# Performance work log

Hardware: AMD Instinct MI355X
Metric: run time of the kernel (lower is better)

Reference implementation:

```python
import jax, jax.numpy as jnp
import numpy as np

D_K = 128
SCALER = np.sqrt(D_K).astype(np.float32)

def setup_inputs() -> dict:
    key = jax.random.key(0)
    kq, kk, kv = jax.random.split(key, 3)
    B, L, D = 16, 2048, D_K
    q = jax.random.normal(kq, (B, L, D), dtype=jnp.float32)
    k = jax.random.normal(kk, (B, L, D), dtype=jnp.float32)
    v = jax.random.normal(kv, (B, L, D), dtype=jnp.float32)
    return {"q": q, "k": k, "v": v}

def reference(q, k, v):
    # score[b, i, j] = q[b, i, :] . k[b, j, :] / sqrt(d_k)
    score = jnp.einsum('bid,bjd->bij', q, k) / SCALER
    attn = jax.nn.softmax(score, axis=-1)
    # output[b, i, :] = sum_j attn[b, i, j] * v[b, j, :]
    return jnp.einsum('bij,bjd->bid', attn, v)
```

## Files before the change

kernel.cpp:

```cpp
#include <hip/hip_runtime.h>
#include <stdint.h>


typedef short bf16x8 __attribute__((ext_vector_type(8)));
typedef float f32x4 __attribute__((ext_vector_type(4)));
typedef unsigned int u32;
typedef unsigned short u16;

#define L_SEQ  2048
#define D_HEAD 128
#define NIT    16
#define TSZ    8388608u
#define PART_SZ (512u * 32768u)
#define LSUM_OFF (2u * TSZ + PART_SZ)
#define WS_NEED (LSUM_OFF + 512u * 128u * 4u)

__device__ __forceinline__ unsigned pk2(float lo, float hi) {
    union { float f; unsigned u; } a, b;
    a.f = lo; b.f = hi;
    return __builtin_amdgcn_perm(b.u + 0x8000u, a.u + 0x8000u, 0x07060302u);
}
__device__ __forceinline__ float ex2(float x) { return __builtin_amdgcn_exp2f(x); }
__device__ __forceinline__ float bflo(unsigned w) {
    union { unsigned u; float f; } v; v.u = w << 16; return v.f;
}
__device__ __forceinline__ float bfhi(unsigned w) {
    union { unsigned u; float f; } v; v.u = w & 0xffff0000u; return v.f;
}
__device__ __forceinline__ void gl_lds16(const u16* g, u16* l) {
    __builtin_amdgcn_global_load_lds(
        (const __attribute__((address_space(1))) u32*)g,
        (__attribute__((address_space(3))) u32*)l, 16, 0, 0);
}

__global__ __launch_bounds__(256, 4)
void prepass(const float* __restrict__ K, const float* __restrict__ V,
             u16* __restrict__ kb, u16* __restrict__ vt) {
    const int id = blockIdx.x, t = threadIdx.x;
    if (id < 512) {
        const float* src = K + (size_t)id * 64 * 128;
        u16*        dst = kb + (size_t)id * 64 * 128;
        const int r = t >> 2;
        #pragma unroll
        for (int i = 0; i < 4; ++i) {
            int gp = (t & 3) * 4 + i;
            int gs = gp ^ (r & 7);
            const float* s = src + r * 128 + gs * 8;
            float4 x0 = *(const float4*)s, x1 = *(const float4*)(s + 4);
            uint4 w;
            w.x = pk2(x0.x, x0.y); w.y = pk2(x0.z, x0.w);
            w.z = pk2(x1.x, x1.y); w.w = pk2(x1.z, x1.w);
            *(uint4*)(dst + r * 128 + gp * 8) = w;
        }
    } else {
        __shared__ float vl[64 * 132];
        const int bid = id - 512;
        const float* src = V + (size_t)bid * 64 * 128;
        {
            int r = t >> 2, c0 = (t & 3) * 32;
            #pragma unroll
            for (int j = 0; j < 8; ++j)
                *(float4*)(&vl[r * 132 + c0 + j * 4]) =
                    *(const float4*)(src + r * 128 + c0 + j * 4);
        }
        __syncthreads();
        u16* dst = vt + (size_t)bid * 8192;
        const int d = t >> 1;
        #pragma unroll
        for (int i = 0; i < 4; ++i) {
            int gp = (t & 1) * 4 + i;
            int kvb = (gp ^ (d & 7)) * 8;
            float p[8];
            #pragma unroll
            for (int j = 0; j < 8; ++j) p[j] = vl[(kvb + j) * 132 + d];
            uint4 w;
            w.x = pk2(p[0], p[1]); w.y = pk2(p[2], p[3]);
            w.z = pk2(p[4], p[5]); w.w = pk2(p[6], p[7]);
            *(uint4*)(dst + d * 64 + gp * 8) = w;
        }
    }
}

__global__ __launch_bounds__(256, 2)
void attn_split(const float* __restrict__ Qg, const u16* __restrict__ kb,
                const u16* __restrict__ vt, u16* __restrict__ part,
                float* __restrict__ lsum) {
    __shared__ __align__(16) char smem[51200];
    const int tid = threadIdx.x;
    const int wv = tid >> 6, lane = tid & 63;
    const int c = lane & 15, qd = lane >> 4, cx = c & 7;
    const int bid = blockIdx.x;
    const int p = bid >> 1, kvh = bid & 1;
    const int b = p & 15, qblk = p >> 4;

    const float* Qp = Qg + (size_t)b * L_SEQ * D_HEAD;
    const u16*   Kp = kb + (size_t)b * L_SEQ * D_HEAD + (size_t)kvh * 1024 * 128;
    const u16*   Vp = vt + (size_t)b * 32 * 8192 + (size_t)kvh * 16 * 8192;
    u16* Kl = (u16*)smem;
    u16* Vl = (u16*)(smem + 16384);
    u16* Pl = (u16*)(smem + 32768) + wv * 2304;

    const int so = wv * 2048 + lane * 8;

    #pragma unroll
    for (int i = 0; i < 4; ++i) {
        gl_lds16(Kp + so + i * 512, Kl + so + i * 512);
        gl_lds16(Vp + so + i * 512, Vl + so + i * 512);
    }

    const float QS = 1.4426950408889634f / 11.313708498984761f;
    bf16x8 qf[2][4];
    #pragma unroll
    for (int s = 0; s < 2; ++s) {
        const float* qrow = Qp + (size_t)(qblk * 128 + wv * 32 + s * 16 + c) * 128 + qd * 8;
        #pragma unroll
        for (int kt = 0; kt < 4; ++kt) {
            float4 x0 = *(const float4*)(qrow + kt * 32);
            float4 x1 = *(const float4*)(qrow + kt * 32 + 4);
            union { unsigned u[4]; bf16x8 v; } tt;
            tt.u[0] = pk2(x0.x * QS, x0.y * QS);
            tt.u[1] = pk2(x0.z * QS, x0.w * QS);
            tt.u[2] = pk2(x1.x * QS, x1.y * QS);
            tt.u[3] = pk2(x1.z * QS, x1.w * QS);
            qf[s][kt] = tt.v;
        }
    }

    f32x4 acc[2][8];
    #pragma unroll
    for (int s = 0; s < 2; ++s)
        #pragma unroll
        for (int dt = 0; dt < 8; ++dt) acc[s][dt] = (f32x4){0.f, 0.f, 0.f, 0.f};
    float lrun[2] = {0.f, 0.f};

    __syncthreads();

    for (int it = 0; it < NIT; ++it) {
        f32x4 st[4][2];
        #pragma unroll
        for (int v = 0; v < 4; ++v) {
            st[v][0] = (f32x4){0.f, 0.f, 0.f, 0.f};
            st[v][1] = (f32x4){0.f, 0.f, 0.f, 0.f};
        }
        #pragma unroll
        for (int kt = 0; kt < 4; ++kt) {
            const int g = ((kt * 4 + qd) ^ cx) * 8;
            #pragma unroll
            for (int v = 0; v < 4; ++v) {
                bf16x8 a = *(const bf16x8*)(Kl + (v * 16 + c) * 128 + g);
                st[v][0] = __builtin_amdgcn_mfma_f32_16x16x32_bf16(a, qf[0][kt], st[v][0], 0, 0, 0);
                st[v][1] = __builtin_amdgcn_mfma_f32_16x16x32_bf16(a, qf[1][kt], st[v][1], 0, 0, 0);
            }
        }
        __syncthreads();

        if (it + 1 < NIT) {
            const u16* kg = Kp + (size_t)(it + 1) * 8192 + so;
            #pragma unroll
            for (int i = 0; i < 4; ++i) gl_lds16(kg + i * 512, Kl + so + i * 512);
        }

        #pragma unroll
        for (int s = 0; s < 2; ++s) {
            float lsm = 0.f;
            #pragma unroll
            for (int v = 0; v < 4; ++v) {
                float p0 = ex2(st[v][s].x), p1 = ex2(st[v][s].y);
                float p2 = ex2(st[v][s].z), p3 = ex2(st[v][s].w);
                lsm += (p0 + p1) + (p2 + p3);
                uint2 w; w.x = pk2(p0, p1); w.y = pk2(p2, p3);
                *(uint2*)(Pl + (s * 16 + c) * 72 + v * 16 + qd * 4) = w;
            }
            lrun[s] += lsm;
        }
        bf16x8 pf[2][2];
        #pragma unroll
        for (int h = 0; h < 2; ++h)
            #pragma unroll
            for (int s = 0; s < 2; ++s)
                pf[h][s] = *(const bf16x8*)(Pl + (s * 16 + c) * 72 + h * 32 + qd * 8);

        #pragma unroll
        for (int dt = 0; dt < 8; ++dt) {
            #pragma unroll
            for (int h = 0; h < 2; ++h) {
                bf16x8 a = *(const bf16x8*)(Vl + (dt * 16 + c) * 64 + ((h * 4 + qd) ^ cx) * 8);
                acc[0][dt] = __builtin_amdgcn_mfma_f32_16x16x32_bf16(a, pf[h][0], acc[0][dt], 0, 0, 0);
                acc[1][dt] = __builtin_amdgcn_mfma_f32_16x16x32_bf16(a, pf[h][1], acc[1][dt], 0, 0, 0);
            }
        }
        __syncthreads();

        if (it + 1 < NIT) {
            const u16* vg = Vp + (size_t)(it + 1) * 8192 + so;
            #pragma unroll
            for (int i = 0; i < 4; ++i) gl_lds16(vg + i * 512, Vl + so + i * 512);
        }
    }

    float ls[2];
    #pragma unroll
    for (int s = 0; s < 2; ++s) {
        float l = lrun[s];
        l += __shfl_xor(l, 16);
        l += __shfl_xor(l, 32);
        ls[s] = l;
    }
    u16* pb = part + (size_t)bid * 16384;
    #pragma unroll
    for (int s = 0; s < 2; ++s)
        #pragma unroll
        for (int dt = 0; dt < 8; ++dt) {
            f32x4 o = acc[s][dt];
            uint2 w; w.x = pk2(o.x, o.y); w.y = pk2(o.z, o.w);
            *(uint2*)(pb + ((((wv * 2 + s) * 8 + dt) * 64 + lane) << 2)) = w;
        }
    if (qd == 0) {
        lsum[p * 256 + kvh * 128 + wv * 32 + c]      = ls[0];
        lsum[p * 256 + kvh * 128 + wv * 32 + 16 + c] = ls[1];
    }
}

__global__ __launch_bounds__(256, 2)
void combine(const u16* __restrict__ part, const float* __restrict__ lsum,
             float* __restrict__ Og) {
    __shared__ float inv[128];
    __shared__ __align__(16) float Ol[64 * 132];
    const int t = threadIdx.x, p = blockIdx.x;
    const int b = p & 15, qblk = p >> 4;
    if (t < 128) {
        float la = lsum[p * 256 + t], lb = lsum[p * 256 + 128 + t];
        inv[t] = 1.0f / (la + lb);
    }
    const uint2* A = (const uint2*)(part + (size_t)(2 * p) * 16384);
    const uint2* B = (const uint2*)(part + (size_t)(2 * p + 1) * 16384);
    __syncthreads();
    #pragma unroll
    for (int h = 0; h < 2; ++h) {
        #pragma unroll
        for (int i = 0; i < 8; ++i) {
            int slot = i * 256 + t;
            int lc = slot >> 6, lane = slot & 63;
            int gc = h * 32 + lc;
            int s = (lc >> 3) & 1, dt = lc & 7;
            int qd = lane >> 4, c = lane & 15;
            int row = (lc >> 4) * 32 + s * 16 + c;
            int d0 = dt * 16 + qd * 4;
            uint2 wa = A[(size_t)gc * 64 + lane];
            uint2 wb = B[(size_t)gc * 64 + lane];
            float iv = inv[h * 64 + row];
            float4 o;
            o.x = (bflo(wa.x) + bflo(wb.x)) * iv;
            o.y = (bfhi(wa.x) + bfhi(wb.x)) * iv;
            o.z = (bflo(wa.y) + bflo(wb.y)) * iv;
            o.w = (bfhi(wa.y) + bfhi(wb.y)) * iv;
            *(float4*)(&Ol[row * 132 + d0]) = o;
        }
        __syncthreads();
        #pragma unroll
        for (int i = 0; i < 8; ++i) {
            int slot = i * 256 + t;
            int row = slot >> 5, c4 = slot & 31;
            float4 val = *(const float4*)(&Ol[row * 132 + c4 * 4]);
            size_t q = (size_t)b * L_SEQ + qblk * 128 + h * 64 + row;
            *(float4*)(Og + q * D_HEAD + c4 * 4) = val;
        }
        __syncthreads();
    }
}

#define FKST 136
#define FVST 72
#define FPST 72
#define FOST 132
#define FV_OFF  17408
#define FP_OFF  (17408 + 18432)
#define FSMEM   (FP_OFF + 4 * 32 * FPST * 2)

union F4fb { float4 v; float f[4]; };

__global__ __launch_bounds__(256, 1)
void attn_fwd_fb(const float* __restrict__ Qg, const float* __restrict__ Kg,
                 const float* __restrict__ Vg, float* __restrict__ Og) {
    __shared__ __align__(16) char smem[FSMEM];
    unsigned short* Kl = (unsigned short*)(smem);
    unsigned short* Vl = (unsigned short*)(smem + FV_OFF);
    float*          Ol = (float*)smem;

    const int tid  = threadIdx.x;
    const int wv   = tid >> 6;
    const int lane = tid & 63;
    const int c    = lane & 15;
    const int qd   = lane >> 4;
    unsigned short* Pl = (unsigned short*)(smem + FP_OFF) + wv * (32 * FPST);

    const int b  = blockIdx.x & 15;
    const int qb = blockIdx.x >> 4;

    const float* Qb = Qg + (size_t)b * L_SEQ * D_HEAD;
    const float* Kb = Kg + (size_t)b * L_SEQ * D_HEAD;
    const float* Vb = Vg + (size_t)b * L_SEQ * D_HEAD;

    const int krow = tid >> 2, kch = tid & 3;
    const int vcc  = tid & 31, vgk = tid >> 5;

    const float QS = 1.4426950408889634f / 11.313708498984761f;
    bf16x8 qf[2][4];
    #pragma unroll
    for (int s = 0; s < 2; ++s) {
        const float* qrow = Qb + (size_t)(qb * 128 + wv * 32 + s * 16 + c) * D_HEAD + qd * 8;
        #pragma unroll
        for (int kt = 0; kt < 4; ++kt) {
            float4 x0 = *(const float4*)(qrow + kt * 32);
            float4 x1 = *(const float4*)(qrow + kt * 32 + 4);
            union { unsigned u[4]; bf16x8 v; } t;
            t.u[0] = pk2(x0.x * QS, x0.y * QS);
            t.u[1] = pk2(x0.z * QS, x0.w * QS);
            t.u[2] = pk2(x1.x * QS, x1.y * QS);
            t.u[3] = pk2(x1.z * QS, x1.w * QS);
            qf[s][kt] = t.v;
        }
    }

    F4fb kreg[8], vreg[8];
    {
        const float* kp = Kb + (size_t)krow * D_HEAD + kch * 32;
        #pragma unroll
        for (int r = 0; r < 8; ++r) kreg[r].v = *(const float4*)(kp + r * 4);
        const float* vp = Vb + (size_t)(vgk * 8) * D_HEAD + vcc * 4;
        #pragma unroll
        for (int r = 0; r < 8; ++r) vreg[r].v = *(const float4*)(vp + (size_t)r * D_HEAD);
    }

    f32x4 acc[2][8];
    #pragma unroll
    for (int s = 0; s < 2; ++s)
        #pragma unroll
        for (int dt = 0; dt < 8; ++dt) acc[s][dt] = (f32x4){0.f, 0.f, 0.f, 0.f};
    float lrun[2] = {0.f, 0.f};

    for (int it = 0; it < 32; ++it) {
        #pragma unroll
        for (int i = 0; i < 4; ++i) {
            uint4 w;
            w.x = pk2(kreg[2*i].f[0],   kreg[2*i].f[1]);
            w.y = pk2(kreg[2*i].f[2],   kreg[2*i].f[3]);
            w.z = pk2(kreg[2*i+1].f[0], kreg[2*i+1].f[1]);
            w.w = pk2(kreg[2*i+1].f[2], kreg[2*i+1].f[3]);
            *(uint4*)(&Kl[krow * FKST + kch * 32 + i * 8]) = w;
        }
        #pragma unroll
        for (int dd = 0; dd < 4; ++dd) {
            uint4 w;
            w.x = pk2(vreg[0].f[dd], vreg[1].f[dd]);
            w.y = pk2(vreg[2].f[dd], vreg[3].f[dd]);
            w.z = pk2(vreg[4].f[dd], vreg[5].f[dd]);
            w.w = pk2(vreg[6].f[dd], vreg[7].f[dd]);
            *(uint4*)(&Vl[(vcc * 4 + dd) * FVST + vgk * 8]) = w;
        }
        __syncthreads();

        if (it + 1 < 32) {
            const float* kp = Kb + (size_t)((it + 1) * 64 + krow) * D_HEAD + kch * 32;
            #pragma unroll
            for (int r = 0; r < 8; ++r) kreg[r].v = *(const float4*)(kp + r * 4);
            const float* vp = Vb + (size_t)((it + 1) * 64 + vgk * 8) * D_HEAD + vcc * 4;
            #pragma unroll
            for (int r = 0; r < 8; ++r) vreg[r].v = *(const float4*)(vp + (size_t)r * D_HEAD);
        }

        f32x4 st[4][2];
        #pragma unroll
        for (int v = 0; v < 4; ++v) { st[v][0] = (f32x4){0,0,0,0}; st[v][1] = (f32x4){0,0,0,0}; }
        #pragma unroll
        for (int kt = 0; kt < 4; ++kt) {
            #pragma unroll
            for (int v = 0; v < 4; ++v) {
                bf16x8 a = *(const bf16x8*)(&Kl[(v * 16 + c) * FKST + kt * 32 + qd * 8]);
                st[v][0] = __builtin_amdgcn_mfma_f32_16x16x32_bf16(a, qf[0][kt], st[v][0], 0, 0, 0);
                st[v][1] = __builtin_amdgcn_mfma_f32_16x16x32_bf16(a, qf[1][kt], st[v][1], 0, 0, 0);
            }
        }

        #pragma unroll
        for (int s = 0; s < 2; ++s) {
            float lsm = 0.f;
            #pragma unroll
            for (int v = 0; v < 4; ++v) {
                float p0 = ex2(st[v][s].x), p1 = ex2(st[v][s].y);
                float p2 = ex2(st[v][s].z), p3 = ex2(st[v][s].w);
                lsm += (p0 + p1) + (p2 + p3);
                uint2 w; w.x = pk2(p0, p1); w.y = pk2(p2, p3);
                *(uint2*)(&Pl[(s * 16 + c) * FPST + v * 16 + qd * 4]) = w;
            }
            lrun[s] += lsm;
        }
        bf16x8 pf[2][2];
        #pragma unroll
        for (int h = 0; h < 2; ++h)
            #pragma unroll
            for (int s = 0; s < 2; ++s)
                pf[h][s] = *(const bf16x8*)(&Pl[(s * 16 + c) * FPST + h * 32 + qd * 8]);

        #pragma unroll
        for (int dt = 0; dt < 8; ++dt) {
            #pragma unroll
            for (int h = 0; h < 2; ++h) {
                bf16x8 a = *(const bf16x8*)(&Vl[(dt * 16 + c) * FVST + h * 32 + qd * 8]);
                acc[0][dt] = __builtin_amdgcn_mfma_f32_16x16x32_bf16(a, pf[h][0], acc[0][dt], 0, 0, 0);
                acc[1][dt] = __builtin_amdgcn_mfma_f32_16x16x32_bf16(a, pf[h][1], acc[1][dt], 0, 0, 0);
            }
        }
        __syncthreads();
    }

    float inv[2];
    #pragma unroll
    for (int s = 0; s < 2; ++s) {
        float l = lrun[s];
        l += __shfl_xor(l, 16);
        l += __shfl_xor(l, 32);
        inv[s] = 1.0f / l;
    }
    #pragma unroll
    for (int pass = 0; pass < 2; ++pass) {
        if ((wv >> 1) == pass) {
            int rw = (wv & 1) * 32;
            #pragma unroll
            for (int s = 0; s < 2; ++s)
                #pragma unroll
                for (int dt = 0; dt < 8; ++dt) {
                    f32x4 o = acc[s][dt];
                    float4 w = {o.x * inv[s], o.y * inv[s], o.z * inv[s], o.w * inv[s]};
                    *(float4*)(&Ol[(rw + s * 16 + c) * FOST + dt * 16 + qd * 4]) = w;
                }
        }
        __syncthreads();
        #pragma unroll
        for (int i = 0; i < 8; ++i) {
            int idx = i * 256 + tid;
            int row = idx >> 5, c4 = idx & 31;
            float4 val = *(const float4*)(&Ol[row * FOST + c4 * 4]);
            size_t q = (size_t)b * L_SEQ + qb * 128 + pass * 64 + row;
            *(float4*)(Og + q * D_HEAD + c4 * 4) = val;
        }
        __syncthreads();
    }
}

extern "C" void kernel_launch(void* const* d_in, const int* in_sizes, int n_in,
                              void* d_out, int out_size, void* d_ws, size_t ws_size,
                              hipStream_t stream) {
    const float* q = (const float*)d_in[0];
    const float* k = (const float*)d_in[1];
    const float* v = (const float*)d_in[2];
    float* out = (float*)d_out;
    if (ws_size >= (size_t)WS_NEED) {
        u16* kb = (u16*)d_ws;
        u16* vt = (u16*)((char*)d_ws + TSZ);
        u16* part = (u16*)((char*)d_ws + 2 * (size_t)TSZ);
        float* ls = (float*)((char*)d_ws + LSUM_OFF);
        prepass<<<dim3(1024), dim3(256), 0, stream>>>(k, v, kb, vt);
        attn_split<<<dim3(512), dim3(256), 0, stream>>>(q, kb, vt, part, ls);
        combine<<<dim3(256), dim3(256), 0, stream>>>(part, ls, out);
    } else {
        attn_fwd_fb<<<dim3(256), dim3(256), 0, stream>>>(q, k, v, out);
    }
}
```

Before: 142.5 us.

## Use 512-thread attention blocks with 4-way KV split and rewrite V transpose prepass

Adds an attn8 kernel in which each 512-thread block handles 256 query rows against a quarter of the KV sequence, so each K/V tile in LDS is reused by eight waves instead of four. A combine4 kernel merges the four partial outputs. The V transpose in the prepass now packs to bf16 in registers before writing LDS, which halves LDS traffic. The fallback path without a workspace is removed. The risks are heavier partial-result traffic, larger LDS per block and lower occupancy.

```diff
diff --git a/kernel.cpp b/kernel.cpp
--- a/kernel.cpp
+++ b/kernel.cpp
@@ -9,11 +9,13 @@
 
 #define L_SEQ  2048
 #define D_HEAD 128
-#define NIT    16
 #define TSZ    8388608u
-#define PART_SZ (512u * 32768u)
-#define LSUM_OFF (2u * TSZ + PART_SZ)
-#define WS_NEED (LSUM_OFF + 512u * 128u * 4u)
+#define W2_PART (2u * TSZ)
+#define W2_LSUM (W2_PART + 512u * 65536u)
+#define WS_NEED2 (W2_LSUM + 512u * 256u * 4u)
+#define W5_PART (2u * TSZ)
+#define W5_LSUM (W5_PART + 512u * 32768u)
+#define WS_NEED5 (W5_LSUM + 512u * 128u * 4u)
 
 __device__ __forceinline__ unsigned pk2(float lo, float hi) {
     union { float f; unsigned u; } a, b;
@@ -53,31 +55,223 @@
             *(uint4*)(dst + r * 128 + gp * 8) = w;
         }
     } else {
-        __shared__ float vl[64 * 132];
+        __shared__ __align__(16) u16 vl[128 * 72];
         const int bid = id - 512;
         const float* src = V + (size_t)bid * 64 * 128;
-        {
-            int r = t >> 2, c0 = (t & 3) * 32;
-            #pragma unroll
-            for (int j = 0; j < 8; ++j)
-                *(float4*)(&vl[r * 132 + c0 + j * 4]) =
-                    *(const float4*)(src + r * 128 + c0 + j * 4);
+        const int vcc = t & 31, vgk = t >> 5;
+        union { float4 v; float f[4]; } vr[8];
+        const float* vp = src + (size_t)(vgk * 8) * 128 + vcc * 4;
+        #pragma unroll
+        for (int r = 0; r < 8; ++r) vr[r].v = *(const float4*)(vp + (size_t)r * 128);
+        #pragma unroll
+        for (int dd = 0; dd < 4; ++dd) {
+            uint4 w;
+            w.x = pk2(vr[0].f[dd], vr[1].f[dd]);
+            w.y = pk2(vr[2].f[dd], vr[3].f[dd]);
+            w.z = pk2(vr[4].f[dd], vr[5].f[dd]);
+            w.w = pk2(vr[6].f[dd], vr[7].f[dd]);
+            *(uint4*)(&vl[(vcc * 4 + dd) * 72 + vgk * 8]) = w;
         }
         __syncthreads();
         u16* dst = vt + (size_t)bid * 8192;
-        const int d = t >> 1;
         #pragma unroll
         for (int i = 0; i < 4; ++i) {
-            int gp = (t & 1) * 4 + i;
-            int kvb = (gp ^ (d & 7)) * 8;
-            float p[8];
-            #pragma unroll
-            for (int j = 0; j < 8; ++j) p[j] = vl[(kvb + j) * 132 + d];
-            uint4 w;
-            w.x = pk2(p[0], p[1]); w.y = pk2(p[2], p[3]);
-            w.z = pk2(p[4], p[5]); w.w = pk2(p[6], p[7]);
-            *(uint4*)(dst + d * 64 + gp * 8) = w;
-        }
+            int flat = t + 256 * i;
+            int d = flat >> 3, gp = flat & 7;
+            uint4 w = *(const uint4*)(&vl[d * 72 + ((gp ^ (d & 7)) * 8)]);
+            *(uint4*)(dst + (size_t)flat * 8) = w;
+        }
+    }
+}
+
+__global__ __launch_bounds__(512, 4)
+void attn8(const float* __restrict__ Qg, const u16* __restrict__ kb,
+           const u16* __restrict__ vt, u16* __restrict__ part,
+           float* __restrict__ lsum) {
+    __shared__ __align__(16) char smem[69632];
+    const int tid = threadIdx.x;
+    const int wv = tid >> 6, lane = tid & 63;
+    const int c = lane & 15, qd = lane >> 4, cx = c & 7;
+    const int bid = blockIdx.x;
+    const int p = bid >> 2, kvh = bid & 3;
+    const int b = p & 15, qblk = p >> 4;
+
+    const float* Qp = Qg + (size_t)b * L_SEQ * D_HEAD;
+    const u16*   Kp = kb + (size_t)b * L_SEQ * D_HEAD + (size_t)kvh * 512 * 128;
+    const u16*   Vp = vt + (size_t)b * 32 * 8192 + (size_t)kvh * 8 * 8192;
+    u16* Kl = (u16*)smem;
+    u16* Vl = (u16*)(smem + 16384);
+    u16* Pl = (u16*)(smem + 32768) + wv * 2304;
+
+    const int so = tid * 8;
+
+    #pragma unroll
+    for (int i = 0; i < 2; ++i) {
+        gl_lds16(Kp + so + i * 4096, Kl + so + i * 4096);
+        gl_lds16(Vp + so + i * 4096, Vl + so + i * 4096);
+    }
+
+    const float QS = 1.4426950408889634f / 11.313708498984761f;
+    bf16x8 qf[2][4];
+    #pragma unroll
+    for (int s = 0; s < 2; ++s) {
+        const float* qrow = Qp + (size_t)(qblk * 256 + wv * 32 + s * 16 + c) * 128 + qd * 8;
+        #pragma unroll
+        for (int kt = 0; kt < 4; ++kt) {
+            float4 x0 = *(const float4*)(qrow + kt * 32);
+            float4 x1 = *(const float4*)(qrow + kt * 32 + 4);
+            union { unsigned u[4]; bf16x8 v; } tt;
+            tt.u[0] = pk2(x0.x * QS, x0.y * QS);
+            tt.u[1] = pk2(x0.z * QS, x0.w * QS);
+            tt.u[2] = pk2(x1.x * QS, x1.y * QS);
+            tt.u[3] = pk2(x1.z * QS, x1.w * QS);
+            qf[s][kt] = tt.v;
+        }
+    }
+
+    f32x4 acc[2][8];
+    #pragma unroll
+    for (int s = 0; s < 2; ++s)
+        #pragma unroll
+        for (int dt = 0; dt < 8; ++dt) acc[s][dt] = (f32x4){0.f, 0.f, 0.f, 0.f};
+    float lrun[2] = {0.f, 0.f};
+
+    __syncthreads();
+
+    for (int it = 0; it < 8; ++it) {
+        f32x4 st[4][2];
+        #pragma unroll
+        for (int v = 0; v < 4; ++v) {
+            st[v][0] = (f32x4){0.f, 0.f, 0.f, 0.f};
+            st[v][1] = (f32x4){0.f, 0.f, 0.f, 0.f};
+        }
+        #pragma unroll
+        for (int kt = 0; kt < 4; ++kt) {
+            const int g = ((kt * 4 + qd) ^ cx) * 8;
+            #pragma unroll
+            for (int v = 0; v < 4; ++v) {
+                bf16x8 a = *(const bf16x8*)(Kl + (v * 16 + c) * 128 + g);
+                st[v][0] = __builtin_amdgcn_mfma_f32_16x16x32_bf16(a, qf[0][kt], st[v][0], 0, 0, 0);
+                st[v][1] = __builtin_amdgcn_mfma_f32_16x16x32_bf16(a, qf[1][kt], st[v][1], 0, 0, 0);
+            }
+        }
+        __syncthreads();
+
+        if (it + 1 < 8) {
+            const u16* kg = Kp + (size_t)(it + 1) * 8192 + so;
+            #pragma unroll
+            for (int i = 0; i < 2; ++i) gl_lds16(kg + i * 4096, Kl + so + i * 4096);
+        }
+
+        #pragma unroll
+        for (int s = 0; s < 2; ++s) {
+            float lsm = 0.f;
+            #pragma unroll
+            for (int v = 0; v < 4; ++v) {
+                float p0 = ex2(st[v][s].x), p1 = ex2(st[v][s].y);
+                float p2 = ex2(st[v][s].z), p3 = ex2(st[v][s].w);
+                lsm += (p0 + p1) + (p2 + p3);
+                uint2 w; w.x = pk2(p0, p1); w.y = pk2(p2, p3);
+                *(uint2*)(Pl + (s * 16 + c) * 72 + v * 16 + qd * 4) = w;
+            }
+            lrun[s] += lsm;
+        }
+        bf16x8 pf[2][2];
+        #pragma unroll
+        for (int h = 0; h < 2; ++h)
+            #pragma unroll
+            for (int s = 0; s < 2; ++s)
+                pf[h][s] = *(const bf16x8*)(Pl + (s * 16 + c) * 72 + h * 32 + qd * 8);
+
+        #pragma unroll
+        for (int dt = 0; dt < 8; ++dt) {
+            #pragma unroll
+            for (int h = 0; h < 2; ++h) {
+                bf16x8 a = *(const bf16x8*)(Vl + (dt * 16 + c) * 64 + ((h * 4 + qd) ^ cx) * 8);
+                acc[0][dt] = __builtin_amdgcn_mfma_f32_16x16x32_bf16(a, pf[h][0], acc[0][dt], 0, 0, 0);
+                acc[1][dt] = __builtin_amdgcn_mfma_f32_16x16x32_bf16(a, pf[h][1], acc[1][dt], 0, 0, 0);
+            }
+        }
+        __syncthreads();
+
+        if (it + 1 < 8) {
+            const u16* vg = Vp + (size_t)(it + 1) * 8192 + so;
+            #pragma unroll
+            for (int i = 0; i < 2; ++i) gl_lds16(vg + i * 4096, Vl + so + i * 4096);
+        }
+    }
+
+    float ls[2];
+    #pragma unroll
+    for (int s = 0; s < 2; ++s) {
+        float l = lrun[s];
+        l += __shfl_xor(l, 16);
+        l += __shfl_xor(l, 32);
+        ls[s] = l;
+    }
+    u16* pb = part + (size_t)bid * 32768;
+    #pragma unroll
+    for (int s = 0; s < 2; ++s)
+        #pragma unroll
+        for (int dt = 0; dt < 8; ++dt) {
+            f32x4 o = acc[s][dt];
+            uint2 w; w.x = pk2(o.x, o.y); w.y = pk2(o.z, o.w);
+            *(uint2*)(pb + ((((wv * 2 + s) * 8 + dt) * 64 + lane) << 2)) = w;
+        }
+    if (qd == 0) {
+        int base = p * 1024 + kvh * 256 + wv * 32;
+        lsum[base + c]      = ls[0];
+        lsum[base + 16 + c] = ls[1];
+    }
+}
+
+__global__ __launch_bounds__(256, 2)
+void combine4(const u16* __restrict__ part, const float* __restrict__ lsum,
+              float* __restrict__ Og) {
+    __shared__ float inv[256];
+    __shared__ __align__(16) float Ol[64 * 132];
+    const int t = threadIdx.x, p = blockIdx.x;
+    const int b = p & 15, qblk = p >> 4;
+    {
+        const float* lp = lsum + p * 1024;
+        inv[t] = 1.0f / (lp[t] + lp[256 + t] + lp[512 + t] + lp[768 + t]);
+    }
+    const uint2* P0 = (const uint2*)(part + (size_t)(4 * p + 0) * 32768);
+    const uint2* P1 = (const uint2*)(part + (size_t)(4 * p + 1) * 32768);
+    const uint2* P2 = (const uint2*)(part + (size_t)(4 * p + 2) * 32768);
+    const uint2* P3 = (const uint2*)(part + (size_t)(4 * p + 3) * 32768);
+    __syncthreads();
+    #pragma unroll
+    for (int h = 0; h < 4; ++h) {
+        #pragma unroll
+        for (int i = 0; i < 8; ++i) {
+            int slot = i * 256 + t;
+            int lc = slot >> 6, lane = slot & 63;
+            int gc = h * 32 + lc;
+            int s = (gc >> 3) & 1, dt = gc & 7;
+            int qd = lane >> 4, c = lane & 15;
+            int row = (lc >> 4) * 32 + s * 16 + c;
+            int d0 = dt * 16 + qd * 4;
+            size_t idx = (size_t)gc * 64 + lane;
+            uint2 w0 = P0[idx], w1 = P1[idx], w2 = P2[idx], w3 = P3[idx];
+            float iv = inv[h * 64 + row];
+            float4 o;
+            o.x = (bflo(w0.x) + bflo(w1.x) + bflo(w2.x) + bflo(w3.x)) * iv;
+            o.y = (bfhi(w0.x) + bfhi(w1.x) + bfhi(w2.x) + bfhi(w3.x)) * iv;
+            o.z = (bflo(w0.y) + bflo(w1.y) + bflo(w2.y) + bflo(w3.y)) * iv;
+            o.w = (bfhi(w0.y) + bfhi(w1.y) + bfhi(w2.y) + bfhi(w3.y)) * iv;
+            *(float4*)(&Ol[row * 132 + d0]) = o;
+        }
+        __syncthreads();
+        #pragma unroll
+        for (int i = 0; i < 8; ++i) {
+            int slot = i * 256 + t;
+            int row = slot >> 5, c4 = slot & 31;
+            float4 val = *(const float4*)(&Ol[row * 132 + c4 * 4]);
+            size_t q = (size_t)b * L_SEQ + qblk * 256 + h * 64 + row;
+            *(float4*)(Og + q * D_HEAD + c4 * 4) = val;
+        }
+        __syncthreads();
     }
 }
 
@@ -135,7 +329,7 @@
 
     __syncthreads();
 
-    for (int it = 0; it < NIT; ++it) {
+    for (int it = 0; it < 16; ++it) {
         f32x4 st[4][2];
         #pragma unroll
         for (int v = 0; v < 4; ++v) {
@@ -154,7 +348,7 @@
         }
         __syncthreads();
 
-        if (it + 1 < NIT) {
+        if (it + 1 < 16) {
             const u16* kg = Kp + (size_t)(it + 1) * 8192 + so;
             #pragma unroll
             for (int i = 0; i < 4; ++i) gl_lds16(kg + i * 512, Kl + so + i * 512);
@@ -191,7 +385,7 @@
         }
         __syncthreads();
 
-        if (it + 1 < NIT) {
+        if (it + 1 < 16) {
             const u16* vg = Vp + (size_t)(it + 1) * 8192 + so;
             #pragma unroll
             for (int i = 0; i < 4; ++i) gl_lds16(vg + i * 512, Vl + so + i * 512);
@@ -222,8 +416,8 @@
 }
 
 __global__ __launch_bounds__(256, 2)
-void combine(const u16* __restrict__ part, const float* __restrict__ lsum,
-             float* __restrict__ Og) {
+void combine2(const u16* __restrict__ part, const float* __restrict__ lsum,
+              float* __restrict__ Og) {
     __shared__ float inv[128];
     __shared__ __align__(16) float Ol[64 * 132];
     const int t = threadIdx.x, p = blockIdx.x;
@@ -269,185 +463,6 @@
     }
 }
 
-#define FKST 136
-#define FVST 72
-#define FPST 72
-#define FOST 132
-#define FV_OFF  17408
-#define FP_OFF  (17408 + 18432)
-#define FSMEM   (FP_OFF + 4 * 32 * FPST * 2)
-
-union F4fb { float4 v; float f[4]; };
-
-__global__ __launch_bounds__(256, 1)
-void attn_fwd_fb(const float* __restrict__ Qg, const float* __restrict__ Kg,
-                 const float* __restrict__ Vg, float* __restrict__ Og) {
-    __shared__ __align__(16) char smem[FSMEM];
-    unsigned short* Kl = (unsigned short*)(smem);
-    unsigned short* Vl = (unsigned short*)(smem + FV_OFF);
-    float*          Ol = (float*)smem;
-
-    const int tid  = threadIdx.x;
-    const int wv   = tid >> 6;
-    const int lane = tid & 63;
-    const int c    = lane & 15;
-    const int qd   = lane >> 4;
-    unsigned short* Pl = (unsigned short*)(smem + FP_OFF) + wv * (32 * FPST);
-
-    const int b  = blockIdx.x & 15;
-    const int qb = blockIdx.x >> 4;
-
-    const float* Qb = Qg + (size_t)b * L_SEQ * D_HEAD;
-    const float* Kb = Kg + (size_t)b * L_SEQ * D_HEAD;
-    const float* Vb = Vg + (size_t)b * L_SEQ * D_HEAD;
-
-    const int krow = tid >> 2, kch = tid & 3;
-    const int vcc  = tid & 31, vgk = tid >> 5;
-
-    const float QS = 1.4426950408889634f / 11.313708498984761f;
-    bf16x8 qf[2][4];
-    #pragma unroll
-    for (int s = 0; s < 2; ++s) {
-        const float* qrow = Qb + (size_t)(qb * 128 + wv * 32 + s * 16 + c) * D_HEAD + qd * 8;
-        #pragma unroll
-        for (int kt = 0; kt < 4; ++kt) {
-            float4 x0 = *(const float4*)(qrow + kt * 32);
-            float4 x1 = *(const float4*)(qrow + kt * 32 + 4);
-            union { unsigned u[4]; bf16x8 v; } t;
-            t.u[0] = pk2(x0.x * QS, x0.y * QS);
-            t.u[1] = pk2(x0.z * QS, x0.w * QS);
-            t.u[2] = pk2(x1.x * QS, x1.y * QS);
-            t.u[3] = pk2(x1.z * QS, x1.w * QS);
-            qf[s][kt] = t.v;
-        }
-    }
-
-    F4fb kreg[8], vreg[8];
-    {
-        const float* kp = Kb + (size_t)krow * D_HEAD + kch * 32;
-        #pragma unroll
-        for (int r = 0; r < 8; ++r) kreg[r].v = *(const float4*)(kp + r * 4);
-        const float* vp = Vb + (size_t)(vgk * 8) * D_HEAD + vcc * 4;
-        #pragma unroll
-        for (int r = 0; r < 8; ++r) vreg[r].v = *(const float4*)(vp + (size_t)r * D_HEAD);
-    }
-
-    f32x4 acc[2][8];
-    #pragma unroll
-    for (int s = 0; s < 2; ++s)
-        #pragma unroll
-        for (int dt = 0; dt < 8; ++dt) acc[s][dt] = (f32x4){0.f, 0.f, 0.f, 0.f};
-    float lrun[2] = {0.f, 0.f};
-
-    for (int it = 0; it < 32; ++it) {
-        #pragma unroll
-        for (int i = 0; i < 4; ++i) {
-            uint4 w;
-            w.x = pk2(kreg[2*i].f[0],   kreg[2*i].f[1]);
-            w.y = pk2(kreg[2*i].f[2],   kreg[2*i].f[3]);
-            w.z = pk2(kreg[2*i+1].f[0], kreg[2*i+1].f[1]);
-            w.w = pk2(kreg[2*i+1].f[2], kreg[2*i+1].f[3]);
-            *(uint4*)(&Kl[krow * FKST + kch * 32 + i * 8]) = w;
-        }
-        #pragma unroll
-        for (int dd = 0; dd < 4; ++dd) {
-            uint4 w;
-            w.x = pk2(vreg[0].f[dd], vreg[1].f[dd]);
-            w.y = pk2(vreg[2].f[dd], vreg[3].f[dd]);
-            w.z = pk2(vreg[4].f[dd], vreg[5].f[dd]);
-            w.w = pk2(vreg[6].f[dd], vreg[7].f[dd]);
-            *(uint4*)(&Vl[(vcc * 4 + dd) * FVST + vgk * 8]) = w;
-        }
-        __syncthreads();
-
-        if (it + 1 < 32) {
-            const float* kp = Kb + (size_t)((it + 1) * 64 + krow) * D_HEAD + kch * 32;
-            #pragma unroll
-            for (int r = 0; r < 8; ++r) kreg[r].v = *(const float4*)(kp + r * 4);
-            const float* vp = Vb + (size_t)((it + 1) * 64 + vgk * 8) * D_HEAD + vcc * 4;
-            #pragma unroll
-            for (int r = 0; r < 8; ++r) vreg[r].v = *(const float4*)(vp + (size_t)r * D_HEAD);
-        }
-
-        f32x4 st[4][2];
-        #pragma unroll
-        for (int v = 0; v < 4; ++v) { st[v][0] = (f32x4){0,0,0,0}; st[v][1] = (f32x4){0,0,0,0}; }
-        #pragma unroll
-        for (int kt = 0; kt < 4; ++kt) {
-            #pragma unroll
-            for (int v = 0; v < 4; ++v) {
-                bf16x8 a = *(const bf16x8*)(&Kl[(v * 16 + c) * FKST + kt * 32 + qd * 8]);
-                st[v][0] = __builtin_amdgcn_mfma_f32_16x16x32_bf16(a, qf[0][kt], st[v][0], 0, 0, 0);
-                st[v][1] = __builtin_amdgcn_mfma_f32_16x16x32_bf16(a, qf[1][kt], st[v][1], 0, 0, 0);
-            }
-        }
-
-        #pragma unroll
-        for (int s = 0; s < 2; ++s) {
-            float lsm = 0.f;
-            #pragma unroll
-            for (int v = 0; v < 4; ++v) {
-                float p0 = ex2(st[v][s].x), p1 = ex2(st[v][s].y);
-                float p2 = ex2(st[v][s].z), p3 = ex2(st[v][s].w);
-                lsm += (p0 + p1) + (p2 + p3);
-                uint2 w; w.x = pk2(p0, p1); w.y = pk2(p2, p3);
-                *(uint2*)(&Pl[(s * 16 + c) * FPST + v * 16 + qd * 4]) = w;
-            }
-            lrun[s] += lsm;
-        }
-        bf16x8 pf[2][2];
-        #pragma unroll
-        for (int h = 0; h < 2; ++h)
-            #pragma unroll
-            for (int s = 0; s < 2; ++s)
-                pf[h][s] = *(const bf16x8*)(&Pl[(s * 16 + c) * FPST + h * 32 + qd * 8]);
-
-        #pragma unroll
-        for (int dt = 0; dt < 8; ++dt) {
-            #pragma unroll
-            for (int h = 0; h < 2; ++h) {
-                bf16x8 a = *(const bf16x8*)(&Vl[(dt * 16 + c) * FVST + h * 32 + qd * 8]);
-                acc[0][dt] = __builtin_amdgcn_mfma_f32_16x16x32_bf16(a, pf[h][0], acc[0][dt], 0, 0, 0);
-                acc[1][dt] = __builtin_amdgcn_mfma_f32_16x16x32_bf16(a, pf[h][1], acc[1][dt], 0, 0, 0);
-            }
-        }
-        __syncthreads();
-    }
-
-    float inv[2];
-    #pragma unroll
-    for (int s = 0; s < 2; ++s) {
-        float l = lrun[s];
-        l += __shfl_xor(l, 16);
-        l += __shfl_xor(l, 32);
-        inv[s] = 1.0f / l;
-    }
-    #pragma unroll
-    for (int pass = 0; pass < 2; ++pass) {
-        if ((wv >> 1) == pass) {
-            int rw = (wv & 1) * 32;
-            #pragma unroll
-            for (int s = 0; s < 2; ++s)
-                #pragma unroll
-                for (int dt = 0; dt < 8; ++dt) {
-                    f32x4 o = acc[s][dt];
-                    float4 w = {o.x * inv[s], o.y * inv[s], o.z * inv[s], o.w * inv[s]};
-                    *(float4*)(&Ol[(rw + s * 16 + c) * FOST + dt * 16 + qd * 4]) = w;
-                }
-        }
-        __syncthreads();
-        #pragma unroll
-        for (int i = 0; i < 8; ++i) {
-            int idx = i * 256 + tid;
-            int row = idx >> 5, c4 = idx & 31;
-            float4 val = *(const float4*)(&Ol[row * FOST + c4 * 4]);
-            size_t q = (size_t)b * L_SEQ + qb * 128 + pass * 64 + row;
-            *(float4*)(Og + q * D_HEAD + c4 * 4) = val;
-        }
-        __syncthreads();
-    }
-}
-
 extern "C" void kernel_launch(void* const* d_in, const int* in_sizes, int n_in,
                               void* d_out, int out_size, void* d_ws, size_t ws_size,
                               hipStream_t stream) {
@@ -455,15 +470,18 @@
     const float* k = (const float*)d_in[1];
     const float* v = (const float*)d_in[2];
     float* out = (float*)d_out;
-    if (ws_size >= (size_t)WS_NEED) {
-        u16* kb = (u16*)d_ws;
-        u16* vt = (u16*)((char*)d_ws + TSZ);
-        u16* part = (u16*)((char*)d_ws + 2 * (size_t)TSZ);
-        float* ls = (float*)((char*)d_ws + LSUM_OFF);
-        prepass<<<dim3(1024), dim3(256), 0, stream>>>(k, v, kb, vt);
+    u16* kb = (u16*)d_ws;
+    u16* vt = (u16*)((char*)d_ws + TSZ);
+    prepass<<<dim3(1024), dim3(256), 0, stream>>>(k, v, kb, vt);
+    if (ws_size >= (size_t)WS_NEED2) {
+        u16* part = (u16*)((char*)d_ws + W2_PART);
+        float* ls = (float*)((char*)d_ws + W2_LSUM);
+        attn8<<<dim3(512), dim3(512), 0, stream>>>(q, kb, vt, part, ls);
+        combine4<<<dim3(128), dim3(256), 0, stream>>>(part, ls, out);
+    } else {
+        u16* part = (u16*)((char*)d_ws + W5_PART);
+        float* ls = (float*)((char*)d_ws + W5_LSUM);
         attn_split<<<dim3(512), dim3(256), 0, stream>>>(q, kb, vt, part, ls);
-        combine<<<dim3(256), dim3(256), 0, stream>>>(part, ls, out);
-    } else {
-        attn_fwd_fb<<<dim3(256), dim3(256), 0, stream>>>(q, k, v, out);
-    }
-}
+        combine2<<<dim3(256), dim3(256), 0, stream>>>(part, ls, out);
+    }
+}
```

Measured after the change: 213.9 us. +50.1%, slower.
